# Kernel optimization log

Hardware: AMD Instinct MI355X
Metric: run time of the kernel (lower is better)

The kernel has to match this reference:

```python
import jax, jax.numpy as jnp
import numpy as np

HOP = 2
N_NODES = 50000
D_FEAT = 64
N_NNZ = 800000
N_QEDGES = 32768


def setup_inputs() -> dict:
    key = jax.random.key(0)
    k1, k2, k3, k4, k5 = jax.random.split(key, 5)
    x = jax.random.normal(k1, (N_NODES, D_FEAT), dtype=jnp.float32)
    # degrees must be strictly positive (reciprocal / rsqrt / sqrt applied)
    deg = 1.0 + 63.0 * jax.random.uniform(k2, (N_NODES, 1), dtype=jnp.float32)
    adj_row = jnp.sort(jax.random.randint(k3, (N_NNZ,), 0, N_NODES, dtype=jnp.int32))
    adj_col = jax.random.randint(k4, (N_NNZ,), 0, N_NODES, dtype=jnp.int32)
    edge = jax.random.randint(k5, (2, N_QEDGES), 0, N_NODES, dtype=jnp.int32)
    return {"x": x, "deg": deg, "adj_row": adj_row, "adj_col": adj_col, "edge": edge}


def reference(x, deg, adj_row, adj_col, edge):
    N, D = x.shape
    degrev = 1.0 / deg                      # [N,1]
    # fused degree feature expansion: [N, 3D]
    x3 = jnp.concatenate((x, x * jax.lax.rsqrt(deg), x * jnp.sqrt(deg)), axis=1)

    def spmm(v):  # unweighted adj_t @ v via gather + segment-sum
        return jax.ops.segment_sum(v[adj_col], adj_row, num_segments=N)

    xs = [x3, degrev * spmm(x3)]
    for _ in range(2, HOP + 1):  # Chebyshev-like recurrence
        xs.append(degrev * spmm(xs[-1]) - xs[-2])
    h = jnp.concatenate(xs, axis=1)              # [N, (hop+1)*3*D]
    h = h.reshape(N, 3 * (HOP + 1), D)           # unflatten(1, (-1, D))
    h = jnp.transpose(h, (0, 2, 1))              # [N, D, 3*(hop+1)]
    return h[edge]                               # [2, E_q, D, 3*(hop+1)]
```

## Files before the change

### kernel.cpp

```cpp
#include <hip/hip_runtime.h>

#define N_NODES 50000
#define D_FEAT 64
#define N_NNZ 800000
#define N_ENT 65536

typedef unsigned int uint32;
typedef unsigned short ushort16;

__device__ __forceinline__ uint32 rne1(float a) {
    uint32 u = __float_as_uint(a);
    return (u + 0x7FFFu + ((u >> 16) & 1u)) >> 16;
}
__device__ __forceinline__ uint32 rne2(float a, float b) {
    return rne1(a) | (rne1(b) << 16);
}
__device__ __forceinline__ float bf_lo(uint32 u) { return __uint_as_float(u << 16); }
__device__ __forceinline__ float bf_hi(uint32 u) { return __uint_as_float(u & 0xFFFF0000u); }
__device__ __forceinline__ void unpack8(const uint4 v, float* f) {
    f[0] = bf_lo(v.x); f[1] = bf_hi(v.x);
    f[2] = bf_lo(v.y); f[3] = bf_hi(v.y);
    f[4] = bf_lo(v.z); f[5] = bf_hi(v.z);
    f[6] = bf_lo(v.w); f[7] = bf_hi(v.w);
}
__device__ __forceinline__ float bf1(ushort16 u) { return __uint_as_float(((uint32)u) << 16); }

__global__ void build_rowptr_scal(const int* __restrict__ adj_row,
                                  const float* __restrict__ deg,
                                  int* __restrict__ row_ptr,
                                  float4* __restrict__ scal,
                                  int nnz, int n) {
    int r = blockIdx.x * blockDim.x + threadIdx.x;
    if (r > n) return;
    int lo = 0, hi = nnz;
    while (lo < hi) {
        int mid = (lo + hi) >> 1;
        if (adj_row[mid] < r) lo = mid + 1; else hi = mid;
    }
    row_ptr[r] = lo;
    if (r < n) {
        float d  = deg[r];
        float sq = sqrtf(d);
        scal[r] = make_float4(1.0f / d, 1.0f / sq, sq, 0.0f);
    }
}

__global__ __launch_bounds__(256) void pack_x(const float2* __restrict__ x2,
                                              uint32* __restrict__ xh, int npair) {
    int i = blockIdx.x * blockDim.x + threadIdx.x;
    if (i >= npair) return;
    float2 v = x2[i];
    xh[i] = rne2(v.x, v.y);
}

__global__ __launch_bounds__(256) void spmm1_kernel(
    const uint4* __restrict__ xh, const float4* __restrict__ scal,
    const int* __restrict__ adj_col, const int* __restrict__ row_ptr,
    uint4* __restrict__ y1h, int n) {
    int wave = threadIdx.x >> 6;
    int t    = threadIdx.x & 63;
    int sub  = t >> 3;
    int f    = t & 7;
    int r    = blockIdx.x * 4 + wave;
    if (r >= n) return;

    int s = row_ptr[r], e = row_ptr[r + 1];
    int cnt = e - s;
    float acc[3][8];
#pragma unroll
    for (int g = 0; g < 3; ++g)
#pragma unroll
        for (int j = 0; j < 8; ++j) acc[g][j] = 0.f;

    int nfull = cnt & ~7;
    for (int i = 0; i < nfull; i += 8) {
        int c = adj_col[s + i + sub];
        float4 sc = scal[c];
        uint4 xv = xh[(size_t)c * 8 + f];
        float xf[8]; unpack8(xv, xf);
#pragma unroll
        for (int j = 0; j < 8; ++j) {
            acc[0][j] += xf[j];
            acc[1][j] += xf[j] * sc.y;
            acc[2][j] += xf[j] * sc.z;
        }
    }
    if (nfull + sub < cnt) {
        int c = adj_col[s + nfull + sub];
        float4 sc = scal[c];
        uint4 xv = xh[(size_t)c * 8 + f];
        float xf[8]; unpack8(xv, xf);
#pragma unroll
        for (int j = 0; j < 8; ++j) {
            acc[0][j] += xf[j];
            acc[1][j] += xf[j] * sc.y;
            acc[2][j] += xf[j] * sc.z;
        }
    }

#pragma unroll
    for (int off = 8; off <= 32; off <<= 1)
#pragma unroll
        for (int g = 0; g < 3; ++g)
#pragma unroll
            for (int j = 0; j < 8; ++j)
                acc[g][j] += __shfl_xor(acc[g][j], off);

    float dr = scal[r].x;
    if (sub < 3) {
        float v[8];
#pragma unroll
        for (int j = 0; j < 8; ++j) v[j] = acc[sub][j] * dr;
        uint4 o = make_uint4(rne2(v[0], v[1]), rne2(v[2], v[3]),
                             rne2(v[4], v[5]), rne2(v[6], v[7]));
        y1h[(size_t)r * 24 + sub * 8 + f] = o;
    }
}

__global__ __launch_bounds__(256) void spmm2_kernel(
    const float4* __restrict__ x4, const float4* __restrict__ scal,
    const int* __restrict__ adj_col, const int* __restrict__ row_ptr,
    const uint4* __restrict__ y1h, uint4* __restrict__ y2h, int n) {
    int wave = threadIdx.x >> 6;
    int t    = threadIdx.x & 63;
    int sub  = t >> 3;
    int f    = t & 7;
    int r    = blockIdx.x * 4 + wave;
    if (r >= n) return;

    int s = row_ptr[r], e = row_ptr[r + 1];
    int cnt = e - s;
    float acc[3][8];
#pragma unroll
    for (int g = 0; g < 3; ++g)
#pragma unroll
        for (int j = 0; j < 8; ++j) acc[g][j] = 0.f;

    int nfull = cnt & ~7;
    for (int i = 0; i < nfull; i += 8) {
        int c = adj_col[s + i + sub];
        const uint4* yc = y1h + (size_t)c * 24;
        uint4 b0 = yc[f], b1 = yc[8 + f], b2 = yc[16 + f];
        float f0[8], f1[8], f2[8];
        unpack8(b0, f0); unpack8(b1, f1); unpack8(b2, f2);
#pragma unroll
        for (int j = 0; j < 8; ++j) {
            acc[0][j] += f0[j]; acc[1][j] += f1[j]; acc[2][j] += f2[j];
        }
    }
    if (nfull + sub < cnt) {
        int c = adj_col[s + nfull + sub];
        const uint4* yc = y1h + (size_t)c * 24;
        uint4 b0 = yc[f], b1 = yc[8 + f], b2 = yc[16 + f];
        float f0[8], f1[8], f2[8];
        unpack8(b0, f0); unpack8(b1, f1); unpack8(b2, f2);
#pragma unroll
        for (int j = 0; j < 8; ++j) {
            acc[0][j] += f0[j]; acc[1][j] += f1[j]; acc[2][j] += f2[j];
        }
    }

#pragma unroll
    for (int off = 8; off <= 32; off <<= 1)
#pragma unroll
        for (int g = 0; g < 3; ++g)
#pragma unroll
            for (int j = 0; j < 8; ++j)
                acc[g][j] += __shfl_xor(acc[g][j], off);

    float4 sc = scal[r];
    if (sub < 3) {
        float w = (sub == 0) ? 1.0f : (sub == 1) ? sc.y : sc.z;
        float4 xa = x4[(size_t)r * 16 + f * 2];
        float4 xb = x4[(size_t)r * 16 + f * 2 + 1];
        float xr[8] = {xa.x, xa.y, xa.z, xa.w, xb.x, xb.y, xb.z, xb.w};
        float v[8];
#pragma unroll
        for (int j = 0; j < 8; ++j) v[j] = sc.x * acc[sub][j] - xr[j] * w;
        uint4 o = make_uint4(rne2(v[0], v[1]), rne2(v[2], v[3]),
                             rne2(v[4], v[5]), rne2(v[6], v[7]));
        y2h[(size_t)r * 24 + sub * 8 + f] = o;
    }
}

__global__ __launch_bounds__(256) void gather_kernel(
    const float* __restrict__ x, const float4* __restrict__ scal,
    const int* __restrict__ edge, const ushort16* __restrict__ y1h,
    const ushort16* __restrict__ y2h, float* __restrict__ out) {
    __shared__ __align__(16) float lds[4][576];
    int wave = threadIdx.x >> 6;
    int t    = threadIdx.x & 63;
    int ent  = blockIdx.x * 4 + wave;

    int n = edge[ent];
    float4 sc = scal[n];
    float xv = x[n * D_FEAT + t];
    const ushort16* y1n = y1h + (size_t)n * 192;
    const ushort16* y2n = y2h + (size_t)n * 192;

    float h[9];
    h[0] = xv;              h[1] = xv * sc.y;       h[2] = xv * sc.z;
    h[3] = bf1(y1n[t]);     h[4] = bf1(y1n[64 + t]); h[5] = bf1(y1n[128 + t]);
    h[6] = bf1(y2n[t]);     h[7] = bf1(y2n[64 + t]); h[8] = bf1(y2n[128 + t]);

#pragma unroll
    for (int g = 0; g < 9; ++g) lds[wave][t * 9 + g] = h[g];
    __syncthreads();

    const float4* l4 = (const float4*)lds[wave];
    float4* o4 = (float4*)(out + (size_t)ent * 576);
    o4[t]      = l4[t];
    o4[t + 64] = l4[t + 64];
    if (t < 16) o4[t + 128] = l4[t + 128];
}

extern "C" void kernel_launch(void* const* d_in, const int* in_sizes, int n_in,
                              void* d_out, int out_size, void* d_ws, size_t ws_size,
                              hipStream_t stream) {
    const float* x       = (const float*)d_in[0];
    const float* deg     = (const float*)d_in[1];
    const int*   adj_row = (const int*)d_in[2];
    const int*   adj_col = (const int*)d_in[3];
    const int*   edge    = (const int*)d_in[4];
    float* out = (float*)d_out;

    char* ws = (char*)d_ws;
    size_t off = 0;
    int*    row_ptr = (int*)ws;            off = ((size_t)(N_NODES + 1) * 4 + 255) & ~(size_t)255;
    float4* scal    = (float4*)(ws + off); off += (size_t)N_NODES * 16;
    uint32* xh      = (uint32*)(ws + off); off += (size_t)N_NODES * 64 * 2;
    off = (off + 255) & ~(size_t)255;
    uint4*  y1h     = (uint4*)(ws + off);  off += (size_t)N_NODES * 192 * 2;
    off = (off + 255) & ~(size_t)255;
    uint4*  y2h     = (uint4*)(ws + off);

    build_rowptr_scal<<<(N_NODES + 1 + 255) / 256, 256, 0, stream>>>(
        adj_row, deg, row_ptr, scal, N_NNZ, N_NODES);
    pack_x<<<(N_NODES * 32 + 255) / 256, 256, 0, stream>>>(
        (const float2*)x, xh, N_NODES * 32);
    spmm1_kernel<<<(N_NODES + 3) / 4, 256, 0, stream>>>(
        (const uint4*)xh, scal, adj_col, row_ptr, y1h, N_NODES);
    spmm2_kernel<<<(N_NODES + 3) / 4, 256, 0, stream>>>(
        (const float4*)x, scal, adj_col, row_ptr, y1h, y2h, N_NODES);
    gather_kernel<<<N_ENT / 4, 256, 0, stream>>>(
        x, scal, edge, (const ushort16*)y1h, (const ushort16*)y2h, out);
}
```

Baseline: 296.0 us.

## Map one row per 8-lane group in SpMM kernels, removing cross-lane reductions

Both SpMM kernels now give each 8-lane group its own row instead of giving each wave one row, so a wave handles 8 rows at once. Each group walks its row's neighbours sequentially, unrolled by two, and the three shuffle-reduction stages plus the idle-lane stores disappear. Every lane now writes all three output channel groups. The cost is load imbalance across the 8 rows in a wave, which have varying degrees, and less memory-level parallelism per row.

```diff
diff --git a/kernel.cpp b/kernel.cpp
--- a/kernel.cpp
+++ b/kernel.cpp
@@ -57,130 +57,123 @@
     const uint4* __restrict__ xh, const float4* __restrict__ scal,
     const int* __restrict__ adj_col, const int* __restrict__ row_ptr,
     uint4* __restrict__ y1h, int n) {
-    int wave = threadIdx.x >> 6;
     int t    = threadIdx.x & 63;
-    int sub  = t >> 3;
     int f    = t & 7;
-    int r    = blockIdx.x * 4 + wave;
+    int r    = (blockIdx.x * 4 + (threadIdx.x >> 6)) * 8 + (t >> 3);
     if (r >= n) return;
 
     int s = row_ptr[r], e = row_ptr[r + 1];
     int cnt = e - s;
-    float acc[3][8];
-#pragma unroll
-    for (int g = 0; g < 3; ++g)
-#pragma unroll
-        for (int j = 0; j < 8; ++j) acc[g][j] = 0.f;
-
-    int nfull = cnt & ~7;
-    for (int i = 0; i < nfull; i += 8) {
-        int c = adj_col[s + i + sub];
+    float a0[8], a1[8], a2[8];
+#pragma unroll
+    for (int j = 0; j < 8; ++j) { a0[j] = 0.f; a1[j] = 0.f; a2[j] = 0.f; }
+
+    int i = 0;
+    for (; i + 2 <= cnt; i += 2) {
+        int c0 = adj_col[s + i];
+        int c1 = adj_col[s + i + 1];
+        uint4 xv0 = xh[(size_t)c0 * 8 + f];
+        uint4 xv1 = xh[(size_t)c1 * 8 + f];
+        float4 sc0 = scal[c0];
+        float4 sc1 = scal[c1];
+        float xf0[8], xf1[8];
+        unpack8(xv0, xf0); unpack8(xv1, xf1);
+#pragma unroll
+        for (int j = 0; j < 8; ++j) {
+            a0[j] += xf0[j];
+            a1[j] += xf0[j] * sc0.y;
+            a2[j] += xf0[j] * sc0.z;
+            a0[j] += xf1[j];
+            a1[j] += xf1[j] * sc1.y;
+            a2[j] += xf1[j] * sc1.z;
+        }
+    }
+    if (i < cnt) {
+        int c = adj_col[s + i];
+        uint4 xv = xh[(size_t)c * 8 + f];
         float4 sc = scal[c];
-        uint4 xv = xh[(size_t)c * 8 + f];
         float xf[8]; unpack8(xv, xf);
 #pragma unroll
         for (int j = 0; j < 8; ++j) {
-            acc[0][j] += xf[j];
-            acc[1][j] += xf[j] * sc.y;
-            acc[2][j] += xf[j] * sc.z;
-        }
-    }
-    if (nfull + sub < cnt) {
-        int c = adj_col[s + nfull + sub];
-        float4 sc = scal[c];
-        uint4 xv = xh[(size_t)c * 8 + f];
-        float xf[8]; unpack8(xv, xf);
-#pragma unroll
-        for (int j = 0; j < 8; ++j) {
-            acc[0][j] += xf[j];
-            acc[1][j] += xf[j] * sc.y;
-            acc[2][j] += xf[j] * sc.z;
-        }
-    }
-
-#pragma unroll
-    for (int off = 8; off <= 32; off <<= 1)
-#pragma unroll
-        for (int g = 0; g < 3; ++g)
-#pragma unroll
-            for (int j = 0; j < 8; ++j)
-                acc[g][j] += __shfl_xor(acc[g][j], off);
+            a0[j] += xf[j];
+            a1[j] += xf[j] * sc.y;
+            a2[j] += xf[j] * sc.z;
+        }
+    }
 
     float dr = scal[r].x;
-    if (sub < 3) {
-        float v[8];
-#pragma unroll
-        for (int j = 0; j < 8; ++j) v[j] = acc[sub][j] * dr;
-        uint4 o = make_uint4(rne2(v[0], v[1]), rne2(v[2], v[3]),
-                             rne2(v[4], v[5]), rne2(v[6], v[7]));
-        y1h[(size_t)r * 24 + sub * 8 + f] = o;
-    }
+    uint4* yr = y1h + (size_t)r * 24 + f;
+    yr[0]  = make_uint4(rne2(a0[0]*dr, a0[1]*dr), rne2(a0[2]*dr, a0[3]*dr),
+                        rne2(a0[4]*dr, a0[5]*dr), rne2(a0[6]*dr, a0[7]*dr));
+    yr[8]  = make_uint4(rne2(a1[0]*dr, a1[1]*dr), rne2(a1[2]*dr, a1[3]*dr),
+                        rne2(a1[4]*dr, a1[5]*dr), rne2(a1[6]*dr, a1[7]*dr));
+    yr[16] = make_uint4(rne2(a2[0]*dr, a2[1]*dr), rne2(a2[2]*dr, a2[3]*dr),
+                        rne2(a2[4]*dr, a2[5]*dr), rne2(a2[6]*dr, a2[7]*dr));
 }
 
 __global__ __launch_bounds__(256) void spmm2_kernel(
     const float4* __restrict__ x4, const float4* __restrict__ scal,
     const int* __restrict__ adj_col, const int* __restrict__ row_ptr,
     const uint4* __restrict__ y1h, uint4* __restrict__ y2h, int n) {
-    int wave = threadIdx.x >> 6;
     int t    = threadIdx.x & 63;
-    int sub  = t >> 3;
     int f    = t & 7;
-    int r    = blockIdx.x * 4 + wave;
+    int r    = (blockIdx.x * 4 + (threadIdx.x >> 6)) * 8 + (t >> 3);
     if (r >= n) return;
 
     int s = row_ptr[r], e = row_ptr[r + 1];
     int cnt = e - s;
-    float acc[3][8];
-#pragma unroll
-    for (int g = 0; g < 3; ++g)
-#pragma unroll
-        for (int j = 0; j < 8; ++j) acc[g][j] = 0.f;
-
-    int nfull = cnt & ~7;
-    for (int i = 0; i < nfull; i += 8) {
-        int c = adj_col[s + i + sub];
-        const uint4* yc = y1h + (size_t)c * 24;
-        uint4 b0 = yc[f], b1 = yc[8 + f], b2 = yc[16 + f];
+    float a0[8], a1[8], a2[8];
+#pragma unroll
+    for (int j = 0; j < 8; ++j) { a0[j] = 0.f; a1[j] = 0.f; a2[j] = 0.f; }
+
+    int i = 0;
+    for (; i + 2 <= cnt; i += 2) {
+        int c0 = adj_col[s + i];
+        int c1 = adj_col[s + i + 1];
+        const uint4* yc0 = y1h + (size_t)c0 * 24 + f;
+        const uint4* yc1 = y1h + (size_t)c1 * 24 + f;
+        uint4 b0 = yc0[0], b1 = yc0[8], b2 = yc0[16];
+        uint4 d0 = yc1[0], d1 = yc1[8], d2 = yc1[16];
+        float f0[8], f1[8], f2[8], g0[8], g1[8], g2[8];
+        unpack8(b0, f0); unpack8(b1, f1); unpack8(b2, f2);
+        unpack8(d0, g0); unpack8(d1, g1); unpack8(d2, g2);
+#pragma unroll
+        for (int j = 0; j < 8; ++j) {
+            a0[j] += f0[j] + g0[j];
+            a1[j] += f1[j] + g1[j];
+            a2[j] += f2[j] + g2[j];
+        }
+    }
+    if (i < cnt) {
+        int c = adj_col[s + i];
+        const uint4* yc = y1h + (size_t)c * 24 + f;
+        uint4 b0 = yc[0], b1 = yc[8], b2 = yc[16];
         float f0[8], f1[8], f2[8];
         unpack8(b0, f0); unpack8(b1, f1); unpack8(b2, f2);
 #pragma unroll
         for (int j = 0; j < 8; ++j) {
-            acc[0][j] += f0[j]; acc[1][j] += f1[j]; acc[2][j] += f2[j];
-        }
-    }
-    if (nfull + sub < cnt) {
-        int c = adj_col[s + nfull + sub];
-        const uint4* yc = y1h + (size_t)c * 24;
-        uint4 b0 = yc[f], b1 = yc[8 + f], b2 = yc[16 + f];
-        float f0[8], f1[8], f2[8];
-        unpack8(b0, f0); unpack8(b1, f1); unpack8(b2, f2);
-#pragma unroll
-        for (int j = 0; j < 8; ++j) {
-            acc[0][j] += f0[j]; acc[1][j] += f1[j]; acc[2][j] += f2[j];
-        }
-    }
-
-#pragma unroll
-    for (int off = 8; off <= 32; off <<= 1)
-#pragma unroll
-        for (int g = 0; g < 3; ++g)
-#pragma unroll
-            for (int j = 0; j < 8; ++j)
-                acc[g][j] += __shfl_xor(acc[g][j], off);
+            a0[j] += f0[j]; a1[j] += f1[j]; a2[j] += f2[j];
+        }
+    }
 
     float4 sc = scal[r];
-    if (sub < 3) {
-        float w = (sub == 0) ? 1.0f : (sub == 1) ? sc.y : sc.z;
-        float4 xa = x4[(size_t)r * 16 + f * 2];
-        float4 xb = x4[(size_t)r * 16 + f * 2 + 1];
-        float xr[8] = {xa.x, xa.y, xa.z, xa.w, xb.x, xb.y, xb.z, xb.w};
-        float v[8];
-#pragma unroll
-        for (int j = 0; j < 8; ++j) v[j] = sc.x * acc[sub][j] - xr[j] * w;
-        uint4 o = make_uint4(rne2(v[0], v[1]), rne2(v[2], v[3]),
-                             rne2(v[4], v[5]), rne2(v[6], v[7]));
-        y2h[(size_t)r * 24 + sub * 8 + f] = o;
-    }
+    float4 xa = x4[(size_t)r * 16 + f * 2];
+    float4 xb = x4[(size_t)r * 16 + f * 2 + 1];
+    float xr[8] = {xa.x, xa.y, xa.z, xa.w, xb.x, xb.y, xb.z, xb.w};
+    float v0[8], v1[8], v2[8];
+#pragma unroll
+    for (int j = 0; j < 8; ++j) {
+        v0[j] = sc.x * a0[j] - xr[j];
+        v1[j] = sc.x * a1[j] - xr[j] * sc.y;
+        v2[j] = sc.x * a2[j] - xr[j] * sc.z;
+    }
+    uint4* yr = y2h + (size_t)r * 24 + f;
+    yr[0]  = make_uint4(rne2(v0[0], v0[1]), rne2(v0[2], v0[3]),
+                        rne2(v0[4], v0[5]), rne2(v0[6], v0[7]));
+    yr[8]  = make_uint4(rne2(v1[0], v1[1]), rne2(v1[2], v1[3]),
+                        rne2(v1[4], v1[5]), rne2(v1[6], v1[7]));
+    yr[16] = make_uint4(rne2(v2[0], v2[1]), rne2(v2[2], v2[3]),
+                        rne2(v2[4], v2[5]), rne2(v2[6], v2[7]));
 }
 
 __global__ __launch_bounds__(256) void gather_kernel(
@@ -199,7 +192,7 @@
     const ushort16* y2n = y2h + (size_t)n * 192;
 
     float h[9];
-    h[0] = xv;              h[1] = xv * sc.y;       h[2] = xv * sc.z;
+    h[0] = xv;              h[1] = xv * sc.y;        h[2] = xv * sc.z;
     h[3] = bf1(y1n[t]);     h[4] = bf1(y1n[64 + t]); h[5] = bf1(y1n[128 + t]);
     h[6] = bf1(y2n[t]);     h[7] = bf1(y2n[64 + t]); h[8] = bf1(y2n[128 + t]);
 
@@ -238,9 +231,9 @@
         adj_row, deg, row_ptr, scal, N_NNZ, N_NODES);
     pack_x<<<(N_NODES * 32 + 255) / 256, 256, 0, stream>>>(
         (const float2*)x, xh, N_NODES * 32);
-    spmm1_kernel<<<(N_NODES + 3) / 4, 256, 0, stream>>>(
+    spmm1_kernel<<<(N_NODES + 31) / 32, 256, 0, stream>>>(
         (const uint4*)xh, scal, adj_col, row_ptr, y1h, N_NODES);
-    spmm2_kernel<<<(N_NODES + 3) / 4, 256, 0, stream>>>(
+    spmm2_kernel<<<(N_NODES + 31) / 32, 256, 0, stream>>>(
         (const float4*)x, scal, adj_col, row_ptr, y1h, y2h, N_NODES);
     gather_kernel<<<N_ENT / 4, 256, 0, stream>>>(
         x, scal, edge, (const ushort16*)y1h, (const ushort16*)y2h, out);
```

Measured after the change: 257.8 us. 1.15x faster.
